# Kernel optimization log

Measured on AMD Instinct MI355X. Metric: run time of the kernel, lower is better.

## Reference

```python
import jax, jax.numpy as jnp
import numpy as np

EMBED_DIM = 512
NUM = 1
N_GROUPS = 4
STEP = 4
MAX_N = 3072
SCALE_DIM = EMBED_DIM // NUM            # 512 (e passed to get_mask)
NEW_DIM = SCALE_DIM * N_GROUPS          # 2048 (q/k projection width)
SCALING = NEW_DIM ** -0.5


def build_sparse_mask(n, e, n_groups, step):
    """Replicates MultiheadSparseReluAttention.get_mask: bool mask (n, e*n_groups),
    True = masked. Each row keeps a contiguous window of e features; window start
    slides by `step` per row, zig-zagging direction every `row_num` rows."""
    e1 = e * n_groups
    row_num = (e1 - e) // step + 1
    j = np.arange(n)
    local = j % row_num
    block = j // row_num
    start = np.where(block % 2 == 0, local * step, (row_num - 1 - local) * step)
    cols = start[:, None] + np.arange(e)[None, :]
    mask = np.ones((n, e1), dtype=bool)
    mask[j[:, None], cols] = False
    return mask


def setup_inputs() -> dict:
    key = jax.random.key(0)
    ks = jax.random.split(key, 6)
    L, B, E = 2048, 4, EMBED_DIM
    inv_sqrt_e = 1.0 / np.sqrt(E).astype(np.float32)
    return {
        "query": jax.random.normal(ks[0], (L, B, E), jnp.float32),
        "key":   jax.random.normal(ks[1], (L, B, E), jnp.float32),
        "value": jax.random.normal(ks[2], (L, B, E), jnp.float32),
        "q_w": jax.random.normal(ks[3], (NEW_DIM, E), jnp.float32) * inv_sqrt_e,
        "q_b": jnp.zeros((NEW_DIM,), jnp.float32),
        "k_w": jax.random.normal(ks[4], (NEW_DIM, E), jnp.float32) * inv_sqrt_e,
        "k_b": jnp.zeros((NEW_DIM,), jnp.float32),
        "v_w": jax.random.normal(ks[5], (E, E), jnp.float32) * inv_sqrt_e,
        "v_b": jnp.zeros((E,), jnp.float32),
        "feat_mask": jnp.asarray(build_sparse_mask(MAX_N, SCALE_DIM, N_GROUPS, STEP)),
    }


def reference(query, key, value, q_w, q_b, k_w, k_b, v_w, v_b, feat_mask):
    # query/key/value: (L, B, E) time-major as in fairseq
    L = query.shape[0]
    S = key.shape[0]
    q = jax.nn.relu(query @ q_w.T + q_b) * SCALING   # (L, B, new_dim)
    k = jax.nn.relu(key @ k_w.T + k_b)               # (S, B, new_dim)
    v = value @ v_w.T + v_b                          # (S, B, E)
    # structured feature sparsification (mask True -> zero)
    q = jnp.where(feat_mask[:L, None, :], 0.0, q)
    k = jnp.where(feat_mask[:S, None, :], 0.0, k)
    # ReLU attention: no softmax, scores are already non-negative
    attn = jnp.einsum('lbd,sbd->bls', q, k)          # (B, L, S)
    out = jnp.einsum('bls,sbe->lbe', attn, v)        # (L, B, E)
    return out
```

## Files before the change

### kernel.cpp

```cpp
#include <hip/hip_runtime.h>


typedef _Float16 f16x8 __attribute__((ext_vector_type(8)));
typedef float f32x4 __attribute__((ext_vector_type(4)));

#define L_DIM 2048
#define E_DIM 512
#define S_DIM 2048
#define SCALING_C 0.02209708691207961f

__device__ __forceinline__ int win_start(int l) {
    int local = l % 385;
    int blk   = l / 385;
    return ((blk & 1) == 0) ? (local << 2) : ((384 - local) << 2);
}

__device__ __forceinline__ void gload_lds16(const _Float16* g, _Float16* l) {
    __builtin_amdgcn_global_load_lds(
        (const __attribute__((address_space(1))) void*)g,
        (__attribute__((address_space(3))) void*)l, 16, 0, 0);
}

__global__ void cvt_f32_to_f16(const float* __restrict__ in,
                               _Float16* __restrict__ out, int n8) {
    int i = blockIdx.x * 256 + threadIdx.x;
    if (i >= n8) return;
    const float4* p = (const float4*)in + 2 * (size_t)i;
    float4 a = p[0], b = p[1];
    f16x8 o = {(_Float16)a.x, (_Float16)a.y, (_Float16)a.z, (_Float16)a.w,
               (_Float16)b.x, (_Float16)b.y, (_Float16)b.z, (_Float16)b.w};
    *((f16x8*)out + i) = o;
}

__global__ void transpose_v(const _Float16* __restrict__ V,
                            _Float16* __restrict__ Vt) {
    __shared__ _Float16 t[32][33];
    int b  = blockIdx.z;
    int s0 = blockIdx.y * 32, e0 = blockIdx.x * 32;
    int tx = threadIdx.x & 31, ty = threadIdx.x >> 5;
    #pragma unroll
    for (int i = ty; i < 32; i += 8)
        t[i][tx] = V[((size_t)b * S_DIM + s0 + i) * E_DIM + e0 + tx];
    __syncthreads();
    #pragma unroll
    for (int i = ty; i < 32; i += 8)
        Vt[((size_t)b * E_DIM + e0 + i) * S_DIM + s0 + tx] = t[tx][i];
}

template <int MODE>
__global__ __launch_bounds__(256)
void gemm_mfma(const _Float16* __restrict__ A, const _Float16* __restrict__ Bm,
               const float* __restrict__ bias, void* __restrict__ Cout,
               int K, size_t batchA, size_t batchB) {
    __shared__ __align__(16) _Float16 lA[128 * 32];
    __shared__ __align__(16) _Float16 lB[128 * 32];

    const int tid  = threadIdx.x;
    const int lane = tid & 63;
    const int wid  = tid >> 6;
    const int row0 = blockIdx.y * 128;
    const int col0 = blockIdx.x * 128;
    const int z    = blockIdx.z;

    const _Float16* Ab = A + (size_t)z * batchA + (size_t)row0 * K;
    const _Float16* Bb = Bm + (size_t)z * batchB + (size_t)col0 * K;

    const int c0 = tid, c1 = tid + 256;
    const _Float16* srcA0 = Ab + (size_t)(c0 >> 2) * K + ((c0 & 3) << 3);
    const _Float16* srcA1 = Ab + (size_t)(c1 >> 2) * K + ((c1 & 3) << 3);
    const _Float16* srcB0 = Bb + (size_t)(c0 >> 2) * K + ((c0 & 3) << 3);
    const _Float16* srcB1 = Bb + (size_t)(c1 >> 2) * K + ((c1 & 3) << 3);
    _Float16* dA0 = &lA[wid * 512];
    _Float16* dA1 = &lA[2048 + wid * 512];
    _Float16* dB0 = &lB[wid * 512];
    _Float16* dB1 = &lB[2048 + wid * 512];

    const int kgrp = (lane >> 4) << 3;
    const int arow = (wid >> 1) * 64 + (lane & 15);
    const int brow = (wid & 1) * 64 + (lane & 15);

    f32x4 acc[4][4] = {};

    for (int k0 = 0; k0 < K; k0 += 32) {
        gload_lds16(srcA0, dA0);
        gload_lds16(srcA1, dA1);
        gload_lds16(srcB0, dB0);
        gload_lds16(srcB1, dB1);
        srcA0 += 32; srcA1 += 32; srcB0 += 32; srcB1 += 32;
        asm volatile("s_waitcnt vmcnt(0)" ::: "memory");
        __syncthreads();

        f16x8 af[4], bf[4];
        #pragma unroll
        for (int t = 0; t < 4; ++t) {
            af[t] = *(const f16x8*)&lA[(arow + t * 16) * 32 + kgrp];
            bf[t] = *(const f16x8*)&lB[(brow + t * 16) * 32 + kgrp];
        }
        #pragma unroll
        for (int mt = 0; mt < 4; ++mt)
            #pragma unroll
            for (int nt = 0; nt < 4; ++nt)
                acc[mt][nt] = __builtin_amdgcn_mfma_f32_16x16x32_f16(
                    af[mt], bf[nt], acc[mt][nt], 0, 0, 0);
        __syncthreads();
    }

    const int colb  = col0 + (wid & 1) * 64 + (lane & 15);
    const int rowb  = row0 + (wid >> 1) * 64 + ((lane >> 4) << 2);
    #pragma unroll
    for (int mt = 0; mt < 4; ++mt) {
        #pragma unroll
        for (int nt = 0; nt < 4; ++nt) {
            f32x4 a = acc[mt][nt];
            int col = colb + nt * 16;
            #pragma unroll
            for (int j = 0; j < 4; ++j) {
                int row = rowb + mt * 16 + j;
                float v = a[j];
                if constexpr (MODE == 2) {
                    v += bias[col];
                    int s = row >> 2, bb = row & 3;
                    ((_Float16*)Cout)[(((size_t)bb * S_DIM + s) << 9) + col] =
                        (_Float16)v;
                } else {
                    ((float*)Cout)[(((size_t)row << 2) + z) * 512 + col] = v;
                }
            }
        }
    }
}

#define STAGE_H(b_, mat_, h_, j_) \
    gload_lds16(src[mat_][h_][j_], \
                &sm[b_][mat_][(h_) * 8192 + wid * 1024 + (j_) * 512])
#define ADV() do { \
    src[0][0][0] += 64; src[0][0][1] += 64; src[0][1][0] += 64; src[0][1][1] += 64; \
    src[1][0][0] += 64; src[1][0][1] += 64; src[1][1][0] += 64; src[1][1][1] += 64; \
} while (0)

template <int MODE>
__global__ __launch_bounds__(512, 2)
void gemm256(const _Float16* __restrict__ A, const _Float16* __restrict__ Bm,
             const float* __restrict__ bias, void* __restrict__ Cout,
             int K, size_t batchA, size_t batchB, int nbx, int nby) {
    __shared__ __align__(16) _Float16 sm[2][2][16384];

    const int nwg  = gridDim.x;
    const int orig = blockIdx.x;
    const int swz  = (orig & 7) * (nwg >> 3) + (orig >> 3);
    const int bx   = swz % nbx;
    const int rem  = swz / nbx;
    const int by   = rem % nby;
    const int z    = rem / nby;

    const int tid  = threadIdx.x;
    const int lane = tid & 63;
    const int wid  = tid >> 6;
    const int wr   = wid >> 2;
    const int wc   = wid & 3;
    const int row0 = by << 8, col0 = bx << 8;

    const _Float16* Ab = A + (size_t)z * batchA + (size_t)row0 * K;
    const _Float16* Bb = Bm + (size_t)z * batchB + (size_t)col0 * K;

    const _Float16* src[2][2][2];
    #pragma unroll
    for (int h = 0; h < 2; ++h)
        #pragma unroll
        for (int j = 0; j < 2; ++j) {
            const int c  = wid * 128 + j * 64 + lane;
            const int r  = c >> 3;
            const int sc = ((lane & 7) ^ (r & 7)) << 3;
            src[0][h][j] = Ab + (size_t)(h * 128 + r) * K + sc;
            src[1][h][j] = Bb + (size_t)(h * 128 + r) * K + sc;
        }

    STAGE_H(0, 0, 0, 0); STAGE_H(0, 0, 0, 1); STAGE_H(0, 0, 1, 0); STAGE_H(0, 0, 1, 1);
    STAGE_H(0, 1, 0, 0); STAGE_H(0, 1, 0, 1); STAGE_H(0, 1, 1, 0); STAGE_H(0, 1, 1, 1);
    ADV();
    asm volatile("s_waitcnt vmcnt(0)" ::: "memory");
    __builtin_amdgcn_s_barrier();

    f32x4 acc[8][4] = {};
    const int q4   = lane >> 4;
    const int sl0  = ((q4 ^ (lane & 7)) << 4);
    const int sl1  = (((4 + q4) ^ (lane & 7)) << 4);
    const int aoff = (wr * 128 + (lane & 15)) * 128;
    const int boff = (wc * 64 + (lane & 15)) * 128;
    const int NT   = K >> 6;

    for (int t = 0; t < NT; ++t) {
        const int  cur = t & 1, nxt = cur ^ 1;
        const bool pre = (t + 1 < NT);
        const char* bA = (const char*)&sm[cur][0][0];
        const char* bB = (const char*)&sm[cur][1][0];

        f16x8 bf[4][2];
        #pragma unroll
        for (int p = 0; p < 4; ++p) {
            if (p == 0) {
                #pragma unroll
                for (int n = 0; n < 4; ++n) {
                    bf[n][0] = *(const f16x8*)(bB + boff + n * 2048 + sl0);
                    bf[n][1] = *(const f16x8*)(bB + boff + n * 2048 + sl1);
                }
            }
            f16x8 a00 = *(const f16x8*)(bA + aoff + (2 * p) * 2048 + sl0);
            f16x8 a01 = *(const f16x8*)(bA + aoff + (2 * p) * 2048 + sl1);
            f16x8 a10 = *(const f16x8*)(bA + aoff + (2 * p + 1) * 2048 + sl0);
            f16x8 a11 = *(const f16x8*)(bA + aoff + (2 * p + 1) * 2048 + sl1);
            if (pre) {
                if (p == 0) { STAGE_H(nxt, 0, 0, 0); STAGE_H(nxt, 0, 0, 1);
                              STAGE_H(nxt, 0, 1, 0); STAGE_H(nxt, 0, 1, 1); }
                if (p == 1) { STAGE_H(nxt, 1, 0, 0); STAGE_H(nxt, 1, 0, 1);
                              STAGE_H(nxt, 1, 1, 0); STAGE_H(nxt, 1, 1, 1); ADV(); }
            }
            __builtin_amdgcn_s_barrier();
            __builtin_amdgcn_s_setprio(1);
            #pragma unroll
            for (int i = 0; i < 2; ++i) {
                f16x8 a0 = (i == 0) ? a00 : a10;
                f16x8 a1 = (i == 0) ? a01 : a11;
                #pragma unroll
                for (int n = 0; n < 4; ++n) {
                    acc[2 * p + i][n] = __builtin_amdgcn_mfma_f32_16x16x32_f16(
                        a0, bf[n][0], acc[2 * p + i][n], 0, 0, 0);
                    acc[2 * p + i][n] = __builtin_amdgcn_mfma_f32_16x16x32_f16(
                        a1, bf[n][1], acc[2 * p + i][n], 0, 0, 0);
                }
            }
            __builtin_amdgcn_s_setprio(0);
            if (p == 3 && pre) asm volatile("s_waitcnt vmcnt(0)" ::: "memory");
            __builtin_amdgcn_s_barrier();
        }
    }

    const int colg = col0 + wc * 64 + (lane & 15);
    const int rowg = row0 + wr * 128 + q4 * 4;
    float bv[4];
    if constexpr (MODE == 0 || MODE == 1) {
        #pragma unroll
        for (int n = 0; n < 4; ++n) bv[n] = bias[colg + n * 16];
    }
    #pragma unroll
    for (int m = 0; m < 8; ++m) {
        #pragma unroll
        for (int n = 0; n < 4; ++n) {
            const int col = colg + n * 16;
            #pragma unroll
            for (int jj = 0; jj < 4; ++jj) {
                const int row = rowg + m * 16 + jj;
                float v = acc[m][n][jj];
                if constexpr (MODE == 0 || MODE == 1) {
                    v = fmaxf(v + bv[n], 0.f);
                    if constexpr (MODE == 0) v *= SCALING_C;
                    const int l = row >> 2, bb = row & 3;
                    const int st = win_start(l);
                    if (col < st || col >= st + 512) v = 0.f;
                    ((_Float16*)Cout)[(((size_t)bb * L_DIM + l) << 11) + col] =
                        (_Float16)v;
                } else {
                    ((_Float16*)Cout)[(size_t)z * 4194304 +
                                      ((size_t)row << 11) + col] = (_Float16)v;
                }
            }
        }
    }
}

extern "C" void kernel_launch(void* const* d_in, const int* in_sizes, int n_in,
                              void* d_out, int out_size, void* d_ws,
                              size_t ws_size, hipStream_t stream) {
    const float* query = (const float*)d_in[0];
    const float* key_i = (const float*)d_in[1];
    const float* value = (const float*)d_in[2];
    const float* q_w   = (const float*)d_in[3];
    const float* q_b   = (const float*)d_in[4];
    const float* k_w   = (const float*)d_in[5];
    const float* k_b   = (const float*)d_in[6];
    const float* v_w   = (const float*)d_in[7];
    const float* v_b   = (const float*)d_in[8];

    _Float16* ws  = (_Float16*)d_ws;
    _Float16* qx  = ws;
    _Float16* kx  = qx + 4194304;
    _Float16* vx  = kx + 4194304;
    _Float16* qwf = vx + 4194304;
    _Float16* kwf = qwf + 1048576;
    _Float16* vwf = kwf + 1048576;
    _Float16* Qb  = vwf + 262144;
    _Float16* Kb  = Qb + 16777216;
    _Float16* Vb  = Kb + 16777216;
    _Float16* Vt  = Vb + 4194304;
    _Float16* At  = Vt + 4194304;

    cvt_f32_to_f16<<<2048, 256, 0, stream>>>(query, qx, 524288);
    cvt_f32_to_f16<<<2048, 256, 0, stream>>>(key_i, kx, 524288);
    cvt_f32_to_f16<<<2048, 256, 0, stream>>>(value, vx, 524288);
    cvt_f32_to_f16<<<512,  256, 0, stream>>>(q_w, qwf, 131072);
    cvt_f32_to_f16<<<512,  256, 0, stream>>>(k_w, kwf, 131072);
    cvt_f32_to_f16<<<128,  256, 0, stream>>>(v_w, vwf, 32768);

    gemm256<0><<<dim3(256), 512, 0, stream>>>(qx, qwf, q_b, Qb, 512, 0, 0, 8, 32);
    gemm256<1><<<dim3(256), 512, 0, stream>>>(kx, kwf, k_b, Kb, 512, 0, 0, 8, 32);
    gemm_mfma<2><<<dim3(4, 64, 1), 256, 0, stream>>>(vx, vwf, v_b, Vb, 512, 0, 0);

    transpose_v<<<dim3(16, 64, 4), 256, 0, stream>>>(Vb, Vt);

    gemm256<3><<<dim3(256), 512, 0, stream>>>(Qb, Kb, nullptr, At, 2048,
                                              4194304, 4194304, 8, 8);

    gemm_mfma<4><<<dim3(4, 16, 4), 256, 0, stream>>>(At, Vt, nullptr, d_out,
                                                     2048, 4194304, 1048576);
}
```

Baseline: 325.5 us.

## Restructure GEMM pipelining, add pipelined 128-tile GEMM, merge conversion launches

The main 256-tile GEMM drops the per-phase barriers. It now loads A fragments from LDS in a double-buffered register scheme, issues all next-tile global-to-LDS loads early, and waits once per K step. Source pointer bookkeeping is simplified to a single base pointer per matrix. The old simple 128-tile GEMM, used for the V projection and attn@V, is replaced by a swizzled, double-buffered, K=64 pipelined variant. The six conversion launches are merged into two. This aims to cut sync stalls and launch overhead, but relies on barrier removal staying race-free with LDS reuse.

```diff
diff --git a/kernel.cpp b/kernel.cpp
--- a/kernel.cpp
+++ b/kernel.cpp
@@ -21,8 +21,14 @@
         (__attribute__((address_space(3))) void*)l, 16, 0, 0);
 }
 
-__global__ void cvt_f32_to_f16(const float* __restrict__ in,
-                               _Float16* __restrict__ out, int n8) {
+__global__ void cvt3(const float* __restrict__ p0, const float* __restrict__ p1,
+                     const float* __restrict__ p2, _Float16* __restrict__ o0,
+                     _Float16* __restrict__ o1, _Float16* __restrict__ o2,
+                     int n0, int n1, int n2) {
+    const int y = blockIdx.y;
+    const float* in  = (y == 0) ? p0 : (y == 1) ? p1 : p2;
+    _Float16*    out = (y == 0) ? o0 : (y == 1) ? o1 : o2;
+    const int    n8  = (y == 0) ? n0 : (y == 1) ? n1 : n2;
     int i = blockIdx.x * 256 + threadIdx.x;
     if (i >= n8) return;
     const float4* p = (const float4*)in + 2 * (size_t)i;
@@ -47,96 +53,9 @@
         Vt[((size_t)b * E_DIM + e0 + i) * S_DIM + s0 + tx] = t[tx][i];
 }
 
-template <int MODE>
-__global__ __launch_bounds__(256)
-void gemm_mfma(const _Float16* __restrict__ A, const _Float16* __restrict__ Bm,
-               const float* __restrict__ bias, void* __restrict__ Cout,
-               int K, size_t batchA, size_t batchB) {
-    __shared__ __align__(16) _Float16 lA[128 * 32];
-    __shared__ __align__(16) _Float16 lB[128 * 32];
-
-    const int tid  = threadIdx.x;
-    const int lane = tid & 63;
-    const int wid  = tid >> 6;
-    const int row0 = blockIdx.y * 128;
-    const int col0 = blockIdx.x * 128;
-    const int z    = blockIdx.z;
-
-    const _Float16* Ab = A + (size_t)z * batchA + (size_t)row0 * K;
-    const _Float16* Bb = Bm + (size_t)z * batchB + (size_t)col0 * K;
-
-    const int c0 = tid, c1 = tid + 256;
-    const _Float16* srcA0 = Ab + (size_t)(c0 >> 2) * K + ((c0 & 3) << 3);
-    const _Float16* srcA1 = Ab + (size_t)(c1 >> 2) * K + ((c1 & 3) << 3);
-    const _Float16* srcB0 = Bb + (size_t)(c0 >> 2) * K + ((c0 & 3) << 3);
-    const _Float16* srcB1 = Bb + (size_t)(c1 >> 2) * K + ((c1 & 3) << 3);
-    _Float16* dA0 = &lA[wid * 512];
-    _Float16* dA1 = &lA[2048 + wid * 512];
-    _Float16* dB0 = &lB[wid * 512];
-    _Float16* dB1 = &lB[2048 + wid * 512];
-
-    const int kgrp = (lane >> 4) << 3;
-    const int arow = (wid >> 1) * 64 + (lane & 15);
-    const int brow = (wid & 1) * 64 + (lane & 15);
-
-    f32x4 acc[4][4] = {};
-
-    for (int k0 = 0; k0 < K; k0 += 32) {
-        gload_lds16(srcA0, dA0);
-        gload_lds16(srcA1, dA1);
-        gload_lds16(srcB0, dB0);
-        gload_lds16(srcB1, dB1);
-        srcA0 += 32; srcA1 += 32; srcB0 += 32; srcB1 += 32;
-        asm volatile("s_waitcnt vmcnt(0)" ::: "memory");
-        __syncthreads();
-
-        f16x8 af[4], bf[4];
-        #pragma unroll
-        for (int t = 0; t < 4; ++t) {
-            af[t] = *(const f16x8*)&lA[(arow + t * 16) * 32 + kgrp];
-            bf[t] = *(const f16x8*)&lB[(brow + t * 16) * 32 + kgrp];
-        }
-        #pragma unroll
-        for (int mt = 0; mt < 4; ++mt)
-            #pragma unroll
-            for (int nt = 0; nt < 4; ++nt)
-                acc[mt][nt] = __builtin_amdgcn_mfma_f32_16x16x32_f16(
-                    af[mt], bf[nt], acc[mt][nt], 0, 0, 0);
-        __syncthreads();
-    }
-
-    const int colb  = col0 + (wid & 1) * 64 + (lane & 15);
-    const int rowb  = row0 + (wid >> 1) * 64 + ((lane >> 4) << 2);
-    #pragma unroll
-    for (int mt = 0; mt < 4; ++mt) {
-        #pragma unroll
-        for (int nt = 0; nt < 4; ++nt) {
-            f32x4 a = acc[mt][nt];
-            int col = colb + nt * 16;
-            #pragma unroll
-            for (int j = 0; j < 4; ++j) {
-                int row = rowb + mt * 16 + j;
-                float v = a[j];
-                if constexpr (MODE == 2) {
-                    v += bias[col];
-                    int s = row >> 2, bb = row & 3;
-                    ((_Float16*)Cout)[(((size_t)bb * S_DIM + s) << 9) + col] =
-                        (_Float16)v;
-                } else {
-                    ((float*)Cout)[(((size_t)row << 2) + z) * 512 + col] = v;
-                }
-            }
-        }
-    }
-}
-
-#define STAGE_H(b_, mat_, h_, j_) \
-    gload_lds16(src[mat_][h_][j_], \
+#define STAGE256(b_, mat_, h_, j_) \
+    gload_lds16(srcb[mat_] + (size_t)((h_) * 128 + (j_) * 8) * K, \
                 &sm[b_][mat_][(h_) * 8192 + wid * 1024 + (j_) * 512])
-#define ADV() do { \
-    src[0][0][0] += 64; src[0][0][1] += 64; src[0][1][0] += 64; src[0][1][1] += 64; \
-    src[1][0][0] += 64; src[1][0][1] += 64; src[1][1][0] += 64; src[1][1][1] += 64; \
-} while (0)
 
 template <int MODE>
 __global__ __launch_bounds__(512, 2)
@@ -163,21 +82,14 @@
     const _Float16* Ab = A + (size_t)z * batchA + (size_t)row0 * K;
     const _Float16* Bb = Bm + (size_t)z * batchB + (size_t)col0 * K;
 
-    const _Float16* src[2][2][2];
-    #pragma unroll
-    for (int h = 0; h < 2; ++h)
-        #pragma unroll
-        for (int j = 0; j < 2; ++j) {
-            const int c  = wid * 128 + j * 64 + lane;
-            const int r  = c >> 3;
-            const int sc = ((lane & 7) ^ (r & 7)) << 3;
-            src[0][h][j] = Ab + (size_t)(h * 128 + r) * K + sc;
-            src[1][h][j] = Bb + (size_t)(h * 128 + r) * K + sc;
-        }
-
-    STAGE_H(0, 0, 0, 0); STAGE_H(0, 0, 0, 1); STAGE_H(0, 0, 1, 0); STAGE_H(0, 0, 1, 1);
-    STAGE_H(0, 1, 0, 0); STAGE_H(0, 1, 0, 1); STAGE_H(0, 1, 1, 0); STAGE_H(0, 1, 1, 1);
-    ADV();
+    const int rl = wid * 16 + (lane >> 3);
+    const int sc = ((lane & 7) ^ (lane >> 3)) << 3;
+    const _Float16* srcb[2] = { Ab + (size_t)rl * K + sc,
+                                Bb + (size_t)rl * K + sc };
+
+    STAGE256(0, 0, 0, 0); STAGE256(0, 0, 0, 1); STAGE256(0, 0, 1, 0); STAGE256(0, 0, 1, 1);
+    STAGE256(0, 1, 0, 0); STAGE256(0, 1, 0, 1); STAGE256(0, 1, 1, 0); STAGE256(0, 1, 1, 1);
+    srcb[0] += 64; srcb[1] += 64;
     asm volatile("s_waitcnt vmcnt(0)" ::: "memory");
     __builtin_amdgcn_s_barrier();
 
@@ -195,44 +107,47 @@
         const char* bA = (const char*)&sm[cur][0][0];
         const char* bB = (const char*)&sm[cur][1][0];
 
-        f16x8 bf[4][2];
+        f16x8 bf[4][2], a[2][4];
+        #pragma unroll
+        for (int n = 0; n < 4; ++n) {
+            bf[n][0] = *(const f16x8*)(bB + boff + n * 2048 + sl0);
+            bf[n][1] = *(const f16x8*)(bB + boff + n * 2048 + sl1);
+        }
+        a[0][0] = *(const f16x8*)(bA + aoff + 0 * 2048 + sl0);
+        a[0][1] = *(const f16x8*)(bA + aoff + 0 * 2048 + sl1);
+        a[0][2] = *(const f16x8*)(bA + aoff + 1 * 2048 + sl0);
+        a[0][3] = *(const f16x8*)(bA + aoff + 1 * 2048 + sl1);
+        if (pre) { STAGE256(nxt, 0, 0, 0); STAGE256(nxt, 0, 0, 1);
+                   STAGE256(nxt, 0, 1, 0); STAGE256(nxt, 0, 1, 1); }
+
         #pragma unroll
         for (int p = 0; p < 4; ++p) {
-            if (p == 0) {
-                #pragma unroll
-                for (int n = 0; n < 4; ++n) {
-                    bf[n][0] = *(const f16x8*)(bB + boff + n * 2048 + sl0);
-                    bf[n][1] = *(const f16x8*)(bB + boff + n * 2048 + sl1);
-                }
-            }
-            f16x8 a00 = *(const f16x8*)(bA + aoff + (2 * p) * 2048 + sl0);
-            f16x8 a01 = *(const f16x8*)(bA + aoff + (2 * p) * 2048 + sl1);
-            f16x8 a10 = *(const f16x8*)(bA + aoff + (2 * p + 1) * 2048 + sl0);
-            f16x8 a11 = *(const f16x8*)(bA + aoff + (2 * p + 1) * 2048 + sl1);
-            if (pre) {
-                if (p == 0) { STAGE_H(nxt, 0, 0, 0); STAGE_H(nxt, 0, 0, 1);
-                              STAGE_H(nxt, 0, 1, 0); STAGE_H(nxt, 0, 1, 1); }
-                if (p == 1) { STAGE_H(nxt, 1, 0, 0); STAGE_H(nxt, 1, 0, 1);
-                              STAGE_H(nxt, 1, 1, 0); STAGE_H(nxt, 1, 1, 1); ADV(); }
-            }
-            __builtin_amdgcn_s_barrier();
+            if (p < 3) {
+                a[(p + 1) & 1][0] = *(const f16x8*)(bA + aoff + (2 * p + 2) * 2048 + sl0);
+                a[(p + 1) & 1][1] = *(const f16x8*)(bA + aoff + (2 * p + 2) * 2048 + sl1);
+                a[(p + 1) & 1][2] = *(const f16x8*)(bA + aoff + (2 * p + 3) * 2048 + sl0);
+                a[(p + 1) & 1][3] = *(const f16x8*)(bA + aoff + (2 * p + 3) * 2048 + sl1);
+            }
+            if (p == 0 && pre) {
+                STAGE256(nxt, 1, 0, 0); STAGE256(nxt, 1, 0, 1);
+                STAGE256(nxt, 1, 1, 0); STAGE256(nxt, 1, 1, 1);
+                srcb[0] += 64; srcb[1] += 64;
+            }
             __builtin_amdgcn_s_setprio(1);
             #pragma unroll
             for (int i = 0; i < 2; ++i) {
-                f16x8 a0 = (i == 0) ? a00 : a10;
-                f16x8 a1 = (i == 0) ? a01 : a11;
                 #pragma unroll
                 for (int n = 0; n < 4; ++n) {
                     acc[2 * p + i][n] = __builtin_amdgcn_mfma_f32_16x16x32_f16(
-                        a0, bf[n][0], acc[2 * p + i][n], 0, 0, 0);
+                        a[p & 1][2 * i], bf[n][0], acc[2 * p + i][n], 0, 0, 0);
                     acc[2 * p + i][n] = __builtin_amdgcn_mfma_f32_16x16x32_f16(
-                        a1, bf[n][1], acc[2 * p + i][n], 0, 0, 0);
+                        a[p & 1][2 * i + 1], bf[n][1], acc[2 * p + i][n], 0, 0, 0);
                 }
             }
             __builtin_amdgcn_s_setprio(0);
-            if (p == 3 && pre) asm volatile("s_waitcnt vmcnt(0)" ::: "memory");
-            __builtin_amdgcn_s_barrier();
-        }
+        }
+        asm volatile("s_waitcnt vmcnt(0)" ::: "memory");
+        __builtin_amdgcn_s_barrier();
     }
 
     const int colg = col0 + wc * 64 + (lane & 15);
@@ -268,6 +183,127 @@
     }
 }
 
+#define STAGE128(b_, mat_, j_) \
+    gload_lds16(srcb[mat_] + (size_t)((j_) * 32) * K, \
+                &sm[b_][mat_][(j_) * 2048 + wid * 512])
+
+template <int MODE>
+__global__ __launch_bounds__(256, 2)
+void gemm128p(const _Float16* __restrict__ A, const _Float16* __restrict__ Bm,
+              const float* __restrict__ bias, void* __restrict__ Cout,
+              int K, size_t batchA, size_t batchB, int nbx, int nby) {
+    __shared__ __align__(16) _Float16 sm[2][2][8192];
+
+    const int nwg  = gridDim.x;
+    const int orig = blockIdx.x;
+    const int swz  = (orig & 7) * (nwg >> 3) + (orig >> 3);
+    const int bx   = swz % nbx;
+    const int rem  = swz / nbx;
+    const int by   = rem % nby;
+    const int z    = rem / nby;
+
+    const int tid  = threadIdx.x;
+    const int lane = tid & 63;
+    const int wid  = tid >> 6;
+    const int wr   = wid >> 1;
+    const int wc   = wid & 1;
+    const int row0 = by << 7, col0 = bx << 7;
+
+    const _Float16* Ab = A + (size_t)z * batchA + (size_t)row0 * K;
+    const _Float16* Bb = Bm + (size_t)z * batchB + (size_t)col0 * K;
+
+    const int rl = wid * 8 + (lane >> 3);
+    const int sc = ((lane & 7) ^ (lane >> 3)) << 3;
+    const _Float16* srcb[2] = { Ab + (size_t)rl * K + sc,
+                                Bb + (size_t)rl * K + sc };
+
+    STAGE128(0, 0, 0); STAGE128(0, 0, 1); STAGE128(0, 0, 2); STAGE128(0, 0, 3);
+    STAGE128(0, 1, 0); STAGE128(0, 1, 1); STAGE128(0, 1, 2); STAGE128(0, 1, 3);
+    srcb[0] += 64; srcb[1] += 64;
+    asm volatile("s_waitcnt vmcnt(0)" ::: "memory");
+    __builtin_amdgcn_s_barrier();
+
+    f32x4 acc[4][4] = {};
+    const int q4   = lane >> 4;
+    const int sl0  = ((q4 ^ (lane & 7)) << 4);
+    const int sl1  = (((4 + q4) ^ (lane & 7)) << 4);
+    const int aoff = (wr * 64 + (lane & 15)) * 128;
+    const int boff = (wc * 64 + (lane & 15)) * 128;
+    const int NT   = K >> 6;
+
+    for (int t = 0; t < NT; ++t) {
+        const int  cur = t & 1, nxt = cur ^ 1;
+        const bool pre = (t + 1 < NT);
+        const char* bA = (const char*)&sm[cur][0][0];
+        const char* bB = (const char*)&sm[cur][1][0];
+
+        f16x8 bf[4][2], a[2][4];
+        #pragma unroll
+        for (int n = 0; n < 4; ++n) {
+            bf[n][0] = *(const f16x8*)(bB + boff + n * 2048 + sl0);
+            bf[n][1] = *(const f16x8*)(bB + boff + n * 2048 + sl1);
+        }
+        a[0][0] = *(const f16x8*)(bA + aoff + 0 * 2048 + sl0);
+        a[0][1] = *(const f16x8*)(bA + aoff + 0 * 2048 + sl1);
+        a[0][2] = *(const f16x8*)(bA + aoff + 1 * 2048 + sl0);
+        a[0][3] = *(const f16x8*)(bA + aoff + 1 * 2048 + sl1);
+        if (pre) { STAGE128(nxt, 0, 0); STAGE128(nxt, 0, 1);
+                   STAGE128(nxt, 0, 2); STAGE128(nxt, 0, 3); }
+
+        #pragma unroll
+        for (int p = 0; p < 2; ++p) {
+            if (p < 1) {
+                a[1][0] = *(const f16x8*)(bA + aoff + 2 * 2048 + sl0);
+                a[1][1] = *(const f16x8*)(bA + aoff + 2 * 2048 + sl1);
+                a[1][2] = *(const f16x8*)(bA + aoff + 3 * 2048 + sl0);
+                a[1][3] = *(const f16x8*)(bA + aoff + 3 * 2048 + sl1);
+            }
+            if (p == 0 && pre) {
+                STAGE128(nxt, 1, 0); STAGE128(nxt, 1, 1);
+                STAGE128(nxt, 1, 2); STAGE128(nxt, 1, 3);
+                srcb[0] += 64; srcb[1] += 64;
+            }
+            __builtin_amdgcn_s_setprio(1);
+            #pragma unroll
+            for (int i = 0; i < 2; ++i) {
+                #pragma unroll
+                for (int n = 0; n < 4; ++n) {
+                    acc[2 * p + i][n] = __builtin_amdgcn_mfma_f32_16x16x32_f16(
+                        a[p][2 * i], bf[n][0], acc[2 * p + i][n], 0, 0, 0);
+                    acc[2 * p + i][n] = __builtin_amdgcn_mfma_f32_16x16x32_f16(
+                        a[p][2 * i + 1], bf[n][1], acc[2 * p + i][n], 0, 0, 0);
+                }
+            }
+            __builtin_amdgcn_s_setprio(0);
+        }
+        asm volatile("s_waitcnt vmcnt(0)" ::: "memory");
+        __builtin_amdgcn_s_barrier();
+    }
+
+    const int colg = col0 + wc * 64 + (lane & 15);
+    const int rowg = row0 + wr * 64 + q4 * 4;
+    #pragma unroll
+    for (int m = 0; m < 4; ++m) {
+        #pragma unroll
+        for (int n = 0; n < 4; ++n) {
+            const int col = colg + n * 16;
+            #pragma unroll
+            for (int jj = 0; jj < 4; ++jj) {
+                const int row = rowg + m * 16 + jj;
+                float v = acc[m][n][jj];
+                if constexpr (MODE == 2) {
+                    v += bias[col];
+                    const int s = row >> 2, bb = row & 3;
+                    ((_Float16*)Cout)[(((size_t)bb * S_DIM + s) << 9) + col] =
+                        (_Float16)v;
+                } else {
+                    ((float*)Cout)[(((size_t)row << 2) + z) * 512 + col] = v;
+                }
+            }
+        }
+    }
+}
+
 extern "C" void kernel_launch(void* const* d_in, const int* in_sizes, int n_in,
                               void* d_out, int out_size, void* d_ws,
                               size_t ws_size, hipStream_t stream) {
@@ -294,22 +330,20 @@
     _Float16* Vt  = Vb + 4194304;
     _Float16* At  = Vt + 4194304;
 
-    cvt_f32_to_f16<<<2048, 256, 0, stream>>>(query, qx, 524288);
-    cvt_f32_to_f16<<<2048, 256, 0, stream>>>(key_i, kx, 524288);
-    cvt_f32_to_f16<<<2048, 256, 0, stream>>>(value, vx, 524288);
-    cvt_f32_to_f16<<<512,  256, 0, stream>>>(q_w, qwf, 131072);
-    cvt_f32_to_f16<<<512,  256, 0, stream>>>(k_w, kwf, 131072);
-    cvt_f32_to_f16<<<128,  256, 0, stream>>>(v_w, vwf, 32768);
+    cvt3<<<dim3(2048, 3), 256, 0, stream>>>(query, key_i, value, qx, kx, vx,
+                                            524288, 524288, 524288);
+    cvt3<<<dim3(512, 3), 256, 0, stream>>>(q_w, k_w, v_w, qwf, kwf, vwf,
+                                           131072, 131072, 32768);
 
     gemm256<0><<<dim3(256), 512, 0, stream>>>(qx, qwf, q_b, Qb, 512, 0, 0, 8, 32);
     gemm256<1><<<dim3(256), 512, 0, stream>>>(kx, kwf, k_b, Kb, 512, 0, 0, 8, 32);
-    gemm_mfma<2><<<dim3(4, 64, 1), 256, 0, stream>>>(vx, vwf, v_b, Vb, 512, 0, 0);
+    gemm128p<2><<<dim3(256), 256, 0, stream>>>(vx, vwf, v_b, Vb, 512, 0, 0, 4, 64);
 
     transpose_v<<<dim3(16, 64, 4), 256, 0, stream>>>(Vb, Vt);
 
     gemm256<3><<<dim3(256), 512, 0, stream>>>(Qb, Kb, nullptr, At, 2048,
                                               4194304, 4194304, 8, 8);
 
-    gemm_mfma<4><<<dim3(4, 16, 4), 256, 0, stream>>>(At, Vt, nullptr, d_out,
-                                                     2048, 4194304, 1048576);
-}
+    gemm128p<4><<<dim3(256), 256, 0, stream>>>(At, Vt, nullptr, d_out, 2048,
+                                               4194304, 1048576, 4, 16);
+}
```

Result: faster. 277.7 us (-14.7%).
